# Optimization experiments

Measured on AMD Instinct MI355X. Metric: run time of the kernel, lower is better.

Reference implementation:

```python
import jax, jax.numpy as jnp
import numpy as np

B, T, TWO_H = 64, 512, 1024  # batch, prev decoding steps, 2*hidden_dim


def setup_inputs() -> dict:
    key = jax.random.key(0)
    k1, k2, k3 = jax.random.split(key, 3)
    h_d_t = jax.random.normal(k1, (B, TWO_H), dtype=jnp.float32)
    prev_h_dec = jax.random.normal(k2, (B, T, TWO_H), dtype=jnp.float32)
    # nn.Bilinear(2H, 2H, attn_dim=1) weight, trunc_norm_init_std ~ 1e-4 typical
    W = jax.random.normal(k3, (1, TWO_H, TWO_H), dtype=jnp.float32) * 1e-4
    return {"h_d_t": h_d_t, "prev_h_dec": prev_h_dec, "W": W}


def reference(h_d_t, prev_h_dec, W):
    # Bilinear score: s[b,t] = h_d_t[b] @ W[0] @ prev_h_dec[b,t]
    q = jnp.einsum('bd,de->be', h_d_t, W[0])          # (B, 2H) -- one small GEMM
    attn_score = jnp.einsum('be,bte->bt', q, prev_h_dec)  # (B, T)
    alpha_t = jax.nn.softmax(attn_score, axis=1)      # (B, T)
    ct_d = jnp.einsum('bt,btd->bd', alpha_t, prev_h_dec)  # (B, 2H)
    new_prev = jnp.concatenate([prev_h_dec, h_d_t[:, None, :]], axis=1)  # (B, T+1, 2H)
    return (ct_d, new_prev)
```

## Files before the change

kernel.cpp:

```cpp
#include <hip/hip_runtime.h>
#include <math.h>

#define BB    64
#define TT    512
#define TWOH  1024
#define TC    16
#define NCHUNK (TT / TC)
#define NP_STRIDE ((TT + 1) * TWOH)

__global__ __launch_bounds__(256) void k_qgemm(const float* __restrict__ h,
                                               const float* __restrict__ W,
                                               float* __restrict__ q) {
    const int e  = blockIdx.x * 256 + threadIdx.x;
    const int b0 = blockIdx.y * 4;
    const float* __restrict__ h0 = h + b0 * TWOH;
    const float* __restrict__ h1 = h0 + TWOH;
    const float* __restrict__ h2 = h1 + TWOH;
    const float* __restrict__ h3 = h2 + TWOH;
    float a0 = 0.f, a1 = 0.f, a2 = 0.f, a3 = 0.f;
    #pragma unroll 8
    for (int d = 0; d < TWOH; ++d) {
        const float w = W[d * TWOH + e];
        a0 = fmaf(h0[d], w, a0);
        a1 = fmaf(h1[d], w, a1);
        a2 = fmaf(h2[d], w, a2);
        a3 = fmaf(h3[d], w, a3);
    }
    q[(b0 + 0) * TWOH + e] = a0;
    q[(b0 + 1) * TWOH + e] = a1;
    q[(b0 + 2) * TWOH + e] = a2;
    q[(b0 + 3) * TWOH + e] = a3;
}

__global__ __launch_bounds__(256) void k_scores_ct(const float* __restrict__ prev,
                                                   const float* __restrict__ qg,
                                                   float* __restrict__ out_np,
                                                   float* __restrict__ ws_m,
                                                   float* __restrict__ ws_l,
                                                   float* __restrict__ ws_ct) {
    const int c   = blockIdx.x;
    const int b   = blockIdx.y;
    const int t0  = c * TC;
    const int tid = threadIdx.x;
    const int lane = tid & 63;
    const int wid  = tid >> 6;

    __shared__ float s_part[TC][4];
    __shared__ float s_score[TC];

    const float4* __restrict__ prow =
        (const float4*)(prev + (size_t)b * TT * TWOH + (size_t)t0 * TWOH) + tid;
    float4* __restrict__ nprow =
        (float4*)(out_np + (size_t)b * NP_STRIDE + (size_t)t0 * TWOH) + tid;
    const float4 q4 = ((const float4*)(qg + b * TWOH))[tid];

    float4 pv[TC];
    #pragma unroll
    for (int t = 0; t < TC; ++t) {
        float4 v = prow[t * 256];
        pv[t] = v;
        nprow[t * 256] = v;
        float pd = v.x * q4.x + v.y * q4.y + v.z * q4.z + v.w * q4.w;
        #pragma unroll
        for (int off = 32; off > 0; off >>= 1)
            pd += __shfl_xor(pd, off, 64);
        if (lane == 0) s_part[t][wid] = pd;
    }
    __syncthreads();
    if (tid < TC)
        s_score[tid] = s_part[tid][0] + s_part[tid][1] + s_part[tid][2] + s_part[tid][3];
    __syncthreads();

    float m = -INFINITY;
    #pragma unroll
    for (int t = 0; t < TC; ++t) m = fmaxf(m, s_score[t]);
    float l = 0.f;
    float4 ct; ct.x = ct.y = ct.z = ct.w = 0.f;
    #pragma unroll
    for (int t = 0; t < TC; ++t) {
        const float w = __expf(s_score[t] - m);
        l += w;
        ct.x = fmaf(w, pv[t].x, ct.x);
        ct.y = fmaf(w, pv[t].y, ct.y);
        ct.z = fmaf(w, pv[t].z, ct.z);
        ct.w = fmaf(w, pv[t].w, ct.w);
    }
    ((float4*)(ws_ct + ((size_t)b * NCHUNK + c) * TWOH))[tid] = ct;
    if (tid == 0) {
        ws_m[b * NCHUNK + c] = m;
        ws_l[b * NCHUNK + c] = l;
    }
}

__global__ __launch_bounds__(256) void k_finalize(const float* __restrict__ h,
                                                  const float* __restrict__ ws_m,
                                                  const float* __restrict__ ws_l,
                                                  const float* __restrict__ ws_ct,
                                                  float* __restrict__ out_ct,
                                                  float* __restrict__ out_np) {
    const int b   = blockIdx.x;
    const int tid = threadIdx.x;

    float M = -INFINITY;
    #pragma unroll
    for (int i = 0; i < NCHUNK; ++i) M = fmaxf(M, ws_m[b * NCHUNK + i]);

    float coef[NCHUNK];
    float L = 0.f;
    #pragma unroll
    for (int i = 0; i < NCHUNK; ++i) {
        const float e = __expf(ws_m[b * NCHUNK + i] - M);
        coef[i] = e;
        L = fmaf(e, ws_l[b * NCHUNK + i], L);
    }
    const float inv = 1.0f / L;

    float4 acc; acc.x = acc.y = acc.z = acc.w = 0.f;
    #pragma unroll
    for (int i = 0; i < NCHUNK; ++i) {
        const float4 v = ((const float4*)(ws_ct + ((size_t)b * NCHUNK + i) * TWOH))[tid];
        const float cc = coef[i];
        acc.x = fmaf(cc, v.x, acc.x);
        acc.y = fmaf(cc, v.y, acc.y);
        acc.z = fmaf(cc, v.z, acc.z);
        acc.w = fmaf(cc, v.w, acc.w);
    }
    acc.x *= inv; acc.y *= inv; acc.z *= inv; acc.w *= inv;
    ((float4*)(out_ct + b * TWOH))[tid] = acc;

    const float4 hv = ((const float4*)(h + b * TWOH))[tid];
    ((float4*)(out_np + (size_t)b * NP_STRIDE + (size_t)TT * TWOH))[tid] = hv;
}

extern "C" void kernel_launch(void* const* d_in, const int* in_sizes, int n_in,
                              void* d_out, int out_size, void* d_ws, size_t ws_size,
                              hipStream_t stream) {
    const float* h    = (const float*)d_in[0];
    const float* prev = (const float*)d_in[1];
    const float* W    = (const float*)d_in[2];
    float* out    = (float*)d_out;
    float* out_ct = out;
    float* out_np = out + BB * TWOH;

    float* q   = (float*)d_ws;
    float* wsm = q + BB * TWOH;
    float* wsl = wsm + BB * NCHUNK;
    float* wsc = wsl + BB * NCHUNK;

    k_qgemm<<<dim3(4, 16), 256, 0, stream>>>(h, W, q);
    k_scores_ct<<<dim3(NCHUNK, BB), 256, 0, stream>>>(prev, q, out_np, wsm, wsl, wsc);
    k_finalize<<<BB, 256, 0, stream>>>(h, wsm, wsl, wsc, out_ct, out_np);
}
```

Baseline: 316.7 us.

## Split-K the q GEMM across batch rows and widen the finalize grid

The q GEMM now launches one block per batch row, column tile and K slice, with h staged in shared memory and partial sums written to workspace. The score kernel adds the four partial q vectors when it loads q. Finalize is spread over four column tiles per batch row instead of one block per row. The aim is to replace a latency-bound GEMM with few blocks and long serial loops by many short blocks, at the cost of more W re-reads from cache and extra partial-sum traffic.

```diff
diff --git a/kernel.cpp b/kernel.cpp
--- a/kernel.cpp
+++ b/kernel.cpp
@@ -6,34 +6,36 @@
 #define TWOH  1024
 #define TC    16
 #define NCHUNK (TT / TC)
+#define KSPLIT 4
 #define NP_STRIDE ((TT + 1) * TWOH)
+
+typedef float vfloat4 __attribute__((ext_vector_type(4)));
+
 
 __global__ __launch_bounds__(256) void k_qgemm(const float* __restrict__ h,
                                                const float* __restrict__ W,
-                                               float* __restrict__ q) {
-    const int e  = blockIdx.x * 256 + threadIdx.x;
-    const int b0 = blockIdx.y * 4;
-    const float* __restrict__ h0 = h + b0 * TWOH;
-    const float* __restrict__ h1 = h0 + TWOH;
-    const float* __restrict__ h2 = h1 + TWOH;
-    const float* __restrict__ h3 = h2 + TWOH;
-    float a0 = 0.f, a1 = 0.f, a2 = 0.f, a3 = 0.f;
-    #pragma unroll 8
-    for (int d = 0; d < TWOH; ++d) {
-        const float w = W[d * TWOH + e];
-        a0 = fmaf(h0[d], w, a0);
-        a1 = fmaf(h1[d], w, a1);
-        a2 = fmaf(h2[d], w, a2);
-        a3 = fmaf(h3[d], w, a3);
-    }
-    q[(b0 + 0) * TWOH + e] = a0;
-    q[(b0 + 1) * TWOH + e] = a1;
-    q[(b0 + 2) * TWOH + e] = a2;
-    q[(b0 + 3) * TWOH + e] = a3;
+                                               float* __restrict__ qpart) {
+    const int tid = threadIdx.x;
+    const int e   = blockIdx.x * 256 + tid;
+    const int b   = blockIdx.y;
+    const int k   = blockIdx.z;
+    const int d0  = k * (TWOH / KSPLIT);
+
+    __shared__ float sh[TWOH / KSPLIT];
+    sh[tid] = h[b * TWOH + d0 + tid];
+    __syncthreads();
+
+    const float* __restrict__ Wp = W + (size_t)d0 * TWOH + e;
+    float acc = 0.f;
+    #pragma unroll 16
+    for (int d = 0; d < TWOH / KSPLIT; ++d)
+        acc = fmaf(sh[d], Wp[(size_t)d * TWOH], acc);
+
+    qpart[((size_t)k * BB + b) * TWOH + e] = acc;
 }
 
 __global__ __launch_bounds__(256) void k_scores_ct(const float* __restrict__ prev,
-                                                   const float* __restrict__ qg,
+                                                   const float* __restrict__ qpart,
                                                    float* __restrict__ out_np,
                                                    float* __restrict__ ws_m,
                                                    float* __restrict__ ws_l,
@@ -48,16 +50,21 @@
     __shared__ float s_part[TC][4];
     __shared__ float s_score[TC];
 
-    const float4* __restrict__ prow =
-        (const float4*)(prev + (size_t)b * TT * TWOH + (size_t)t0 * TWOH) + tid;
-    float4* __restrict__ nprow =
-        (float4*)(out_np + (size_t)b * NP_STRIDE + (size_t)t0 * TWOH) + tid;
-    const float4 q4 = ((const float4*)(qg + b * TWOH))[tid];
+    const vfloat4* __restrict__ prow =
+        (const vfloat4*)(prev + (size_t)b * TT * TWOH + (size_t)t0 * TWOH) + tid;
+    vfloat4* __restrict__ nprow =
+        (vfloat4*)(out_np + (size_t)b * NP_STRIDE + (size_t)t0 * TWOH) + tid;
 
-    float4 pv[TC];
+    const vfloat4* __restrict__ qp = (const vfloat4*)qpart;
+    vfloat4 q4 = qp[((size_t)0 * BB + b) * 256 + tid]
+               + qp[((size_t)1 * BB + b) * 256 + tid]
+               + qp[((size_t)2 * BB + b) * 256 + tid]
+               + qp[((size_t)3 * BB + b) * 256 + tid];
+
+    vfloat4 pv[TC];
     #pragma unroll
     for (int t = 0; t < TC; ++t) {
-        float4 v = prow[t * 256];
+        vfloat4 v = prow[t * 256];
         pv[t] = v;
         nprow[t * 256] = v;
         float pd = v.x * q4.x + v.y * q4.y + v.z * q4.z + v.w * q4.w;
@@ -75,7 +82,7 @@
     #pragma unroll
     for (int t = 0; t < TC; ++t) m = fmaxf(m, s_score[t]);
     float l = 0.f;
-    float4 ct; ct.x = ct.y = ct.z = ct.w = 0.f;
+    vfloat4 ct = (vfloat4)(0.f);
     #pragma unroll
     for (int t = 0; t < TC; ++t) {
         const float w = __expf(s_score[t] - m);
@@ -85,7 +92,7 @@
         ct.z = fmaf(w, pv[t].z, ct.z);
         ct.w = fmaf(w, pv[t].w, ct.w);
     }
-    ((float4*)(ws_ct + ((size_t)b * NCHUNK + c) * TWOH))[tid] = ct;
+    ((vfloat4*)(ws_ct + ((size_t)b * NCHUNK + c) * TWOH))[tid] = ct;
     if (tid == 0) {
         ws_m[b * NCHUNK + c] = m;
         ws_l[b * NCHUNK + c] = l;
@@ -98,8 +105,9 @@
                                                   const float* __restrict__ ws_ct,
                                                   float* __restrict__ out_ct,
                                                   float* __restrict__ out_np) {
-    const int b   = blockIdx.x;
     const int tid = threadIdx.x;
+    const int e   = blockIdx.x * 256 + tid;
+    const int b   = blockIdx.y;
 
     float M = -INFINITY;
     #pragma unroll
@@ -109,27 +117,20 @@
     float L = 0.f;
     #pragma unroll
     for (int i = 0; i < NCHUNK; ++i) {
-        const float e = __expf(ws_m[b * NCHUNK + i] - M);
-        coef[i] = e;
-        L = fmaf(e, ws_l[b * NCHUNK + i], L);
+        const float ce = __expf(ws_m[b * NCHUNK + i] - M);
+        coef[i] = ce;
+        L = fmaf(ce, ws_l[b * NCHUNK + i], L);
     }
     const float inv = 1.0f / L;
 
-    float4 acc; acc.x = acc.y = acc.z = acc.w = 0.f;
+    const float* __restrict__ cp = ws_ct + (size_t)b * NCHUNK * TWOH + e;
+    float acc = 0.f;
     #pragma unroll
-    for (int i = 0; i < NCHUNK; ++i) {
-        const float4 v = ((const float4*)(ws_ct + ((size_t)b * NCHUNK + i) * TWOH))[tid];
-        const float cc = coef[i];
-        acc.x = fmaf(cc, v.x, acc.x);
-        acc.y = fmaf(cc, v.y, acc.y);
-        acc.z = fmaf(cc, v.z, acc.z);
-        acc.w = fmaf(cc, v.w, acc.w);
-    }
-    acc.x *= inv; acc.y *= inv; acc.z *= inv; acc.w *= inv;
-    ((float4*)(out_ct + b * TWOH))[tid] = acc;
+    for (int i = 0; i < NCHUNK; ++i)
+        acc = fmaf(coef[i], cp[(size_t)i * TWOH], acc);
+    out_ct[b * TWOH + e] = acc * inv;
 
-    const float4 hv = ((const float4*)(h + b * TWOH))[tid];
-    ((float4*)(out_np + (size_t)b * NP_STRIDE + (size_t)TT * TWOH))[tid] = hv;
+    out_np[(size_t)b * NP_STRIDE + (size_t)TT * TWOH + e] = h[b * TWOH + e];
 }
 
 extern "C" void kernel_launch(void* const* d_in, const int* in_sizes, int n_in,
@@ -142,12 +143,12 @@
     float* out_ct = out;
     float* out_np = out + BB * TWOH;
 
-    float* q   = (float*)d_ws;
-    float* wsm = q + BB * TWOH;
-    float* wsl = wsm + BB * NCHUNK;
-    float* wsc = wsl + BB * NCHUNK;
+    float* qpart = (float*)d_ws;
+    float* wsm   = qpart + KSPLIT * BB * TWOH;
+    float* wsl   = wsm + BB * NCHUNK;
+    float* wsc   = wsl + BB * NCHUNK;
 
-    k_qgemm<<<dim3(4, 16), 256, 0, stream>>>(h, W, q);
-    k_scores_ct<<<dim3(NCHUNK, BB), 256, 0, stream>>>(prev, q, out_np, wsm, wsl, wsc);
-    k_finalize<<<BB, 256, 0, stream>>>(h, wsm, wsl, wsc, out_ct, out_np);
+    k_qgemm<<<dim3(4, BB, KSPLIT), 256, 0, stream>>>(h, W, qpart);
+    k_scores_ct<<<dim3(NCHUNK, BB), 256, 0, stream>>>(prev, qpart, out_np, wsm, wsl, wsc);
+    k_finalize<<<dim3(4, BB), 256, 0, stream>>>(h, wsm, wsl, wsc, out_ct, out_np);
 }
```

New measurement: 268.0 us. 15.4% less time.
